# Kernel optimization log

Measured on AMD Instinct MI355X. Metric: run time of the kernel, lower is better.

The kernel has to match this reference:

```python
import jax, jax.numpy as jnp
import numpy as np

jax.config.update("jax_enable_x64", True)  # torch casts to double for matrix_exp

EPS_DIAG = 1e-6


def setup_inputs() -> dict:
    key = jax.random.key(0)
    B, D, NB, S = 32, 128, 8, 128
    ks = jax.random.split(key, 9)
    return {
        "z0r": jax.random.normal(ks[0], (B, D), jnp.float32),
        "z0i": jax.random.normal(ks[1], (B, D), jnp.float32),
        # uniform grid: dt = time_steps[0] = 0.01, diffs == dt (uniform branch)
        "time_steps": (jnp.arange(S, dtype=jnp.float32) + 1.0) * 0.01,
        "k_coeffs": jax.random.normal(ks[2], (B, NB), jnp.float32),
        "r_coeffs": jax.random.normal(ks[3], (B, NB), jnp.float32),
        "alpha": jax.random.normal(ks[4], (B, 1), jnp.float32),
        "beta": jax.random.normal(ks[5], (B, 1), jnp.float32),
        "K_bases": jax.random.normal(ks[6], (NB, D, D), jnp.float32) * 0.01,
        "R_bases": jax.random.normal(ks[7], (NB, D, D), jnp.float32) * 0.01,
    }


def _build_generator(k_coeffs, r_coeffs, alpha, beta, K_bases, R_bases):
    # A = alpha * skew(K_sum) + beta * -(R_sum^T @ R_sum), per batch element
    K_sum = jnp.einsum("bn,nij->bij", k_coeffs, K_bases)
    R_sum = jnp.einsum("bn,nij->bij", r_coeffs, R_bases)
    skew = K_sum - jnp.swapaxes(K_sum, -1, -2)
    neg_gram = -jnp.einsum("bji,bjk->bik", R_sum, R_sum)  # -(R^T @ R)
    return alpha[..., None] * skew + beta[..., None] * neg_gram  # (B, D, D)


def _propagators(A, time_steps, uniform):
    D = A.shape[-1]
    S = time_steps.shape[0]
    if uniform:
        dt = time_steps[0]
        A64 = A.astype(jnp.float64) * dt.astype(jnp.float64) + EPS_DIAG * jnp.eye(D, dtype=jnp.float64)
        M = jax.vmap(jax.scipy.linalg.expm)(A64).astype(jnp.complex64)  # (B, D, D)
        # cumulative matrix powers M, M^2, ..., M^S via O(log S) associative scan
        Ms = jnp.broadcast_to(M[:, None], (M.shape[0], S, D, D))
        props = jax.lax.associative_scan(jnp.matmul, Ms, axis=1)
    else:
        A_t = A[:, None].astype(jnp.float64) * time_steps.astype(jnp.float64)[None, :, None, None]
        props = jax.vmap(jax.vmap(jax.scipy.linalg.expm))(A_t).astype(jnp.complex64)
    return props  # (B, S, D, D)


def reference(z0r, z0i, time_steps, k_coeffs, r_coeffs, alpha, beta, K_bases, R_bases):
    ts = np.asarray(time_steps)
    uniform = ts.shape[0] <= 1 or np.allclose(ts[1:] - ts[:-1], ts[0], atol=1e-6)
    A = _build_generator(k_coeffs, r_coeffs, alpha, beta, K_bases, R_bases)
    props = _propagators(A, time_steps, uniform)
    z = (z0r + 1j * z0i).astype(jnp.complex64)  # (B, D)
    # z_evolved[b, s, o] = sum_i z[b, i] * props[b, s, o, i]
    return jnp.einsum("bi,bsoi->bso", z, props)
```

## Files before the change

### kernel.cpp

```cpp
#include <hip/hip_runtime.h>

#define BATCH   32
#define DIM     128
#define NBASES  8
#define SSTEPS  128
#define LDA     136

typedef __attribute__((ext_vector_type(8)))  short s8v;
typedef __attribute__((ext_vector_type(4)))  short s4v;
typedef __attribute__((ext_vector_type(4)))  float f4v;
typedef __attribute__((ext_vector_type(16))) float f16v;

__device__ __forceinline__ f4v mf(s8v a, s8v b, f4v c) {
    return __builtin_amdgcn_mfma_f32_16x16x32_bf16(a, b, c, 0, 0, 0);
}
__device__ __forceinline__ f16v mf32(s8v a, s8v b, f16v c) {
    return __builtin_amdgcn_mfma_f32_32x32x16_bf16(a, b, c, 0, 0, 0);
}
__device__ __forceinline__ s8v ld8(const short* p) {
    return *reinterpret_cast<const s8v*>(p);
}
__device__ __forceinline__ s4v ld4(const short* p) {
    return *reinterpret_cast<const s4v*>(p);
}
__device__ __forceinline__ void st4(short* p, s4v v) {
    *reinterpret_cast<s4v*>(p) = v;
}
__device__ __forceinline__ float upbf(short h) {
    return __uint_as_float(((unsigned)(unsigned short)h) << 16);
}
__device__ __forceinline__ void splitbf(float v, short& hi, short& lo) {
    const unsigned u = __float_as_uint(v);
    hi = (short)(u >> 16);
    const float fh = __uint_as_float(u & 0xffff0000u);
    lo = (short)(__float_as_uint(v - fh) >> 16);
}

__device__ __forceinline__ void write_out(float* __restrict__ outF, int b, int sidx,
                                          int o, int c, float val,
                                          int interleaved, int out_size)
{
    if (interleaved) {
        const int oi = ((b * SSTEPS + sidx) * DIM + o) * 2 + c;
        if (oi < out_size) outF[oi] = val;
    } else if (c == 0) {
        const int oi = (b * SSTEPS + sidx) * DIM + o;
        if (oi < out_size) outF[oi] = val;
    }
}

template<bool TRO, bool NMO>
__device__ __forceinline__ void mm32(const short* __restrict__ Ah,
                                     const short* __restrict__ Al,
                                     const short* __restrict__ Bh,
                                     const short* __restrict__ Bl,
                                     f16v& acc, f16v& acct,
                                     int mb, int nb, int lane)
{
    const int l31 = lane & 31, koc = (lane >> 5) * 8;
    #pragma unroll
    for (int ks = 0; ks < 8; ++ks) {
        const int ko = ks * 16 + koc;
        const s8v ah = ld8(Ah + (mb + l31) * LDA + ko);
        const s8v al = ld8(Al + (mb + l31) * LDA + ko);
        const s8v bh = ld8(Bh + (nb + l31) * LDA + ko);
        const s8v bl = ld8(Bl + (nb + l31) * LDA + ko);
        if (TRO) {
            acc = mf32(ah, bh, acc);
            acc = mf32(ah, bl, acc);
            acc = mf32(al, bh, acc);
        }
        if (NMO) {
            acct = mf32(bh, ah, acct);
            acct = mf32(bl, ah, acct);
            acct = mf32(bh, al, acct);
        }
    }
}

__global__ __launch_bounds__(256)
void sum_kr(const float* __restrict__ kco, const float* __restrict__ rco,
            const float* __restrict__ KB,  const float* __restrict__ RB,
            float* __restrict__ ws)
{
    const int b = blockIdx.x >> 3, s = blockIdx.x & 7, t = threadIdx.x;
    const int boff = s * 16 * DIM + t * 8;
    const int r = s * 16 + (t >> 4), c = (t & 15) * 8;
    float kc[NBASES], rc[NBASES];
    #pragma unroll
    for (int n = 0; n < NBASES; ++n) {
        kc[n] = kco[b * NBASES + n];
        rc[n] = rco[b * NBASES + n];
    }
    float4 ka = {0.f,0.f,0.f,0.f}, kb4 = {0.f,0.f,0.f,0.f};
    float4 ra = {0.f,0.f,0.f,0.f}, rb4 = {0.f,0.f,0.f,0.f};
    #pragma unroll
    for (int n = 0; n < NBASES; ++n) {
        const float4 k0 = *reinterpret_cast<const float4*>(KB + n * DIM * DIM + boff);
        const float4 k1 = *reinterpret_cast<const float4*>(KB + n * DIM * DIM + boff + 4);
        const float4 r0 = *reinterpret_cast<const float4*>(RB + n * DIM * DIM + boff);
        const float4 r1 = *reinterpret_cast<const float4*>(RB + n * DIM * DIM + boff + 4);
        ka.x += kc[n] * k0.x; ka.y += kc[n] * k0.y; ka.z += kc[n] * k0.z; ka.w += kc[n] * k0.w;
        kb4.x += kc[n] * k1.x; kb4.y += kc[n] * k1.y; kb4.z += kc[n] * k1.z; kb4.w += kc[n] * k1.w;
        ra.x += rc[n] * r0.x; ra.y += rc[n] * r0.y; ra.z += rc[n] * r0.z; ra.w += rc[n] * r0.w;
        rb4.x += rc[n] * r1.x; rb4.y += rc[n] * r1.y; rb4.z += rc[n] * r1.z; rb4.w += rc[n] * r1.w;
    }
    float* Ks  = ws + (size_t)b * DIM * DIM;
    float* KsT = ws + (size_t)BATCH * DIM * DIM + (size_t)b * DIM * DIM;
    float* RsT = ws + (size_t)2 * BATCH * DIM * DIM + (size_t)b * DIM * DIM;
    *reinterpret_cast<float4*>(Ks + boff)     = ka;
    *reinterpret_cast<float4*>(Ks + boff + 4) = kb4;
    const float kv[8] = {ka.x, ka.y, ka.z, ka.w, kb4.x, kb4.y, kb4.z, kb4.w};
    const float rv[8] = {ra.x, ra.y, ra.z, ra.w, rb4.x, rb4.y, rb4.z, rb4.w};
    #pragma unroll
    for (int j = 0; j < 8; ++j) {
        KsT[(c + j) * DIM + r] = kv[j];
        RsT[(c + j) * DIM + r] = rv[j];
    }
}

template<int PRE>
__global__ __launch_bounds__(1024) __attribute__((amdgpu_waves_per_eu(4, 4)))
void htg_mfma(const float* __restrict__ z0r, const float* __restrict__ z0i,
              const float* __restrict__ ts,  const float* __restrict__ kco,
              const float* __restrict__ rco, const float* __restrict__ alp,
              const float* __restrict__ bet, const float* __restrict__ KB,
              const float* __restrict__ RB,  const float* __restrict__ wsum,
              float* __restrict__ outF, int interleaved, int out_size)
{
    __shared__ short nm_hi[DIM * LDA], nm_lo[DIM * LDA];
    __shared__ short tr_hi[DIM * LDA], tr_lo[DIM * LDA];
    __shared__ short ht_hi[32 * LDA],  ht_lo[32 * LDA];

    const int b = blockIdx.x, t = threadIdx.x;
    const int w = t >> 6, lane = t & 63;
    const int l15 = lane & 15, quad = lane >> 4;
    const int l31 = lane & 31, kq = lane >> 5;
    const f4v z4 = {0.f, 0.f, 0.f, 0.f};
    const int mb = (w & 3) * 32, nb = (w >> 2) * 32;

    if (PRE) {
        const float* RsT = wsum + (size_t)2 * BATCH * DIM * DIM + (size_t)b * DIM * DIM;
        #pragma unroll
        for (int q = 0; q < 4; ++q) {
            const int e = q * 4096 + t * 4;
            const float4 rv = *reinterpret_cast<const float4*>(RsT + e);
            const int row = e >> 7, colr = e & 127;
            const float rr[4] = {rv.x, rv.y, rv.z, rv.w};
            s4v h4, l4;
            #pragma unroll
            for (int j = 0; j < 4; ++j) {
                short hi, lo; splitbf(rr[j], hi, lo);
                h4[j] = hi; l4[j] = lo;
            }
            st4(&tr_hi[row * LDA + colr], h4);
            st4(&tr_lo[row * LDA + colr], l4);
        }
        if (t < 2 * DIM) {
            const int c = t >> 7, o = t & 127;
            const float zv = (c == 0) ? z0r[b * DIM + o] : z0i[b * DIM + o];
            short hi, lo; splitbf(zv, hi, lo);
            ht_hi[c * LDA + o] = hi; ht_lo[c * LDA + o] = lo;
        }
    } else {
        float rc[NBASES], kc[NBASES];
        #pragma unroll
        for (int n = 0; n < NBASES; ++n) {
            rc[n] = rco[b * NBASES + n];
            kc[n] = kco[b * NBASES + n];
        }
        #pragma unroll
        for (int q = 0; q < 4; ++q) {
            const int e = q * 4096 + t * 4;
            float4 r4 = {0.f, 0.f, 0.f, 0.f}, k4 = {0.f, 0.f, 0.f, 0.f};
            #pragma unroll
            for (int n = 0; n < NBASES; ++n) {
                const float4 rvv = *reinterpret_cast<const float4*>(RB + n * DIM * DIM + e);
                const float4 kvv = *reinterpret_cast<const float4*>(KB + n * DIM * DIM + e);
                r4.x += rc[n] * rvv.x; r4.y += rc[n] * rvv.y;
                r4.z += rc[n] * rvv.z; r4.w += rc[n] * rvv.w;
                k4.x += kc[n] * kvv.x; k4.y += kc[n] * kvv.y;
                k4.z += kc[n] * kvv.z; k4.w += kc[n] * kvv.w;
            }
            const int r = e >> 7, c = e & 127;
            const float rr[4] = {r4.x, r4.y, r4.z, r4.w};
            const float kk[4] = {k4.x, k4.y, k4.z, k4.w};
            s4v kh, kl;
            #pragma unroll
            for (int j = 0; j < 4; ++j) {
                short hi, lo;
                splitbf(rr[j], hi, lo);
                tr_hi[(c + j) * LDA + r] = hi; tr_lo[(c + j) * LDA + r] = lo;
                splitbf(kk[j], hi, lo);
                kh[j] = hi; kl[j] = lo;
            }
            st4(&nm_hi[r * LDA + c], kh);
            st4(&nm_lo[r * LDA + c], kl);
        }
        if (t < 2 * DIM) {
            const int c = t >> 7, o = t & 127;
            const float zv = (c == 0) ? z0r[b * DIM + o] : z0i[b * DIM + o];
            short hi, lo; splitbf(zv, hi, lo);
            ht_hi[c * LDA + o] = hi; ht_lo[c * LDA + o] = lo;
        }
    }
    __syncthreads();

    f16v acc, acct;
    float xsave[16], xsaveT[16];

    float kd[4][4], kdT[4][4];
    if (PRE) {
        const float* Ks  = wsum + (size_t)b * DIM * DIM;
        const float* KsT = wsum + (size_t)BATCH * DIM * DIM + (size_t)b * DIM * DIM;
        #pragma unroll
        for (int r4 = 0; r4 < 4; ++r4) {
            const int row0 = mb + 8 * r4 + 4 * kq;
            const int col  = nb + l31;
            const int rt0  = nb + 8 * r4 + 4 * kq;
            const int ct   = mb + l31;
            #pragma unroll
            for (int j = 0; j < 4; ++j) {
                kd[r4][j]  = Ks[(row0 + j) * DIM + col] - KsT[(row0 + j) * DIM + col];
                kdT[r4][j] = KsT[(rt0 + j) * DIM + ct]  - Ks[(rt0 + j) * DIM + ct];
            }
        }
    } else {
        #pragma unroll
        for (int r4 = 0; r4 < 4; ++r4) {
            {
                const int row0 = mb + 8 * r4 + 4 * kq;
                const int col  = nb + l31;
                const s4v k2h = ld4(&nm_hi[col * LDA + row0]);
                const s4v k2l = ld4(&nm_lo[col * LDA + row0]);
                #pragma unroll
                for (int j = 0; j < 4; ++j)
                    kd[r4][j] = (upbf(nm_hi[(row0 + j) * LDA + col]) +
                                 upbf(nm_lo[(row0 + j) * LDA + col]))
                              - (upbf(k2h[j]) + upbf(k2l[j]));
            }
            {
                const int rt0 = nb + 8 * r4 + 4 * kq;
                const int ct  = mb + l31;
                const s4v k1h = ld4(&nm_hi[ct * LDA + rt0]);
                const s4v k1l = ld4(&nm_lo[ct * LDA + rt0]);
                #pragma unroll
                for (int j = 0; j < 4; ++j)
                    kdT[r4][j] = (upbf(k1h[j]) + upbf(k1l[j]))
                               - (upbf(nm_hi[(rt0 + j) * LDA + ct]) +
                                  upbf(nm_lo[(rt0 + j) * LDA + ct]));
            }
        }
    }
    #pragma unroll
    for (int i = 0; i < 16; ++i) { acc[i] = 0.f; acct[i] = 0.f; }
    mm32<true, true>(tr_hi, tr_lo, tr_hi, tr_lo, acc, acct, mb, nb, lane);
    __syncthreads();
    {
        const float alpha = alp[b], beta = bet[b], dtf = ts[0];
        #pragma unroll
        for (int r4 = 0; r4 < 4; ++r4) {
            {
                const int row0 = mb + 8 * r4 + 4 * kq;
                const int col  = nb + l31;
                s4v h4, l4;
                #pragma unroll
                for (int j = 0; j < 4; ++j) {
                    float x = (alpha * kd[r4][j] - beta * acc[4 * r4 + j]) * dtf;
                    if (row0 + j == col) x += 1e-6f;
                    xsave[4 * r4 + j] = x;
                    short hi, lo; splitbf(x, hi, lo);
                    h4[j] = hi; l4[j] = lo;
                }
                st4(&tr_hi[col * LDA + row0], h4);
                st4(&tr_lo[col * LDA + row0], l4);
            }
            {
                const int rt0 = nb + 8 * r4 + 4 * kq;
                const int ct  = mb + l31;
                s4v h4, l4;
                #pragma unroll
                for (int j = 0; j < 4; ++j) {
                    float x = (alpha * kdT[r4][j] - beta * acct[4 * r4 + j]) * dtf;
                    if (ct == rt0 + j) x += 1e-6f;
                    xsaveT[4 * r4 + j] = x;
                    short hi, lo; splitbf(x, hi, lo);
                    h4[j] = hi; l4[j] = lo;
                }
                st4(&nm_hi[ct * LDA + rt0], h4);
                st4(&nm_lo[ct * LDA + rt0], l4);
            }
        }
    }
    __syncthreads();

    #pragma unroll
    for (int i = 0; i < 16; ++i) { acc[i] = 0.f; acct[i] = 0.f; }
    mm32<true, true>(nm_hi, nm_lo, tr_hi, tr_lo, acc, acct, mb, nb, lane);
    __syncthreads();
    #pragma unroll
    for (int r4 = 0; r4 < 4; ++r4) {
        {
            const int row0 = mb + 8 * r4 + 4 * kq;
            const int col  = nb + l31;
            s4v h4, l4;
            #pragma unroll
            for (int j = 0; j < 4; ++j) {
                const float m = ((row0 + j == col) ? 1.f : 0.f)
                              + xsave[4 * r4 + j] + 0.5f * acc[4 * r4 + j];
                short hi, lo; splitbf(m, hi, lo);
                h4[j] = hi; l4[j] = lo;
            }
            st4(&tr_hi[col * LDA + row0], h4);
            st4(&tr_lo[col * LDA + row0], l4);
        }
        {
            const int rt0 = nb + 8 * r4 + 4 * kq;
            const int ct  = mb + l31;
            s4v h4, l4;
            #pragma unroll
            for (int j = 0; j < 4; ++j) {
                const float m = ((ct == rt0 + j) ? 1.f : 0.f)
                              + xsaveT[4 * r4 + j] + 0.5f * acct[4 * r4 + j];
                short hi, lo; splitbf(m, hi, lo);
                h4[j] = hi; l4[j] = lo;
            }
            st4(&nm_hi[ct * LDA + rt0], h4);
            st4(&nm_lo[ct * LDA + rt0], l4);
        }
    }
    __syncthreads();

    float arp[4];

    #pragma unroll
    for (int stage = 0; stage < 3; ++stage) {
        const int J = 1 << stage;
        if (stage > 0) {
            const int Jp = J >> 1;
            if (w < 8 && l15 < 2 * Jp) {
                const int o0 = w * 16 + quad * 4;
                const int sidx = (l15 >> 1) + Jp - 1;
                #pragma unroll
                for (int r = 0; r < 4; ++r)
                    write_out(outF, b, sidx, o0 + r, l15 & 1, arp[r],
                              interleaved, out_size);
            }
        }
        f4v ar = z4;
        #pragma unroll
        for (int i = 0; i < 16; ++i) { acc[i] = 0.f; acct[i] = 0.f; }
        if (w < 8) {
            #pragma unroll
            for (int kk = 0; kk < DIM; kk += 32) {
                const int ko = kk + quad * 8;
                const s8v rah = ld8(nm_hi + (w * 16 + l15) * LDA + ko);
                const s8v ral = ld8(nm_lo + (w * 16 + l15) * LDA + ko);
                const s8v rbh = ld8(ht_hi + l15 * LDA + ko);
                const s8v rbl = ld8(ht_lo + l15 * LDA + ko);
                ar = mf(rah, rbh, ar);
                ar = mf(rah, rbl, ar);
                ar = mf(ral, rbh, ar);
            }
        }
        mm32<true, true>(nm_hi, nm_lo, tr_hi, tr_lo, acc, acct, mb, nb, lane);
        __syncthreads();
        if (w < 8 && l15 < 2 * J) {
            const int o0 = w * 16 + quad * 4;
            s4v h4, l4;
            #pragma unroll
            for (int r = 0; r < 4; ++r) {
                short hi, lo; splitbf(ar[r], hi, lo);
                h4[r] = hi; l4[r] = lo;
            }
            st4(&ht_hi[(l15 + 2 * J) * LDA + o0], h4);
            st4(&ht_lo[(l15 + 2 * J) * LDA + o0], l4);
        }
        #pragma unroll
        for (int r = 0; r < 4; ++r) arp[r] = ar[r];
        #pragma unroll
        for (int r4 = 0; r4 < 4; ++r4) {
            {
                const int row0 = mb + 8 * r4 + 4 * kq;
                const int col  = nb + l31;
                s4v h4, l4;
                #pragma unroll
                for (int j = 0; j < 4; ++j) {
                    short hi, lo; splitbf(acc[4 * r4 + j], hi, lo);
                    h4[j] = hi; l4[j] = lo;
                }
                st4(&tr_hi[col * LDA + row0], h4);
                st4(&tr_lo[col * LDA + row0], l4);
            }
            {
                const int rt0 = nb + 8 * r4 + 4 * kq;
                const int ct  = mb + l31;
                s4v h4, l4;
                #pragma unroll
                for (int j = 0; j < 4; ++j) {
                    short hi, lo; splitbf(acct[4 * r4 + j], hi, lo);
                    h4[j] = hi; l4[j] = lo;
                }
                st4(&nm_hi[ct * LDA + rt0], h4);
                st4(&nm_lo[ct * LDA + rt0], l4);
            }
        }
        __syncthreads();
    }

    {
        const int J = 8;
        {
            const int Jp = 4;
            if (w < 8 && l15 < 2 * Jp) {
                const int o0 = w * 16 + quad * 4;
                const int sidx = (l15 >> 1) + Jp - 1;
                #pragma unroll
                for (int r = 0; r < 4; ++r)
                    write_out(outF, b, sidx, o0 + r, l15 & 1, arp[r],
                              interleaved, out_size);
            }
        }
        f4v ar = z4;
        #pragma unroll
        for (int i = 0; i < 16; ++i) acct[i] = 0.f;
        if (w < 8) {
            #pragma unroll
            for (int kk = 0; kk < DIM; kk += 32) {
                const int ko = kk + quad * 8;
                const s8v rah = ld8(nm_hi + (w * 16 + l15) * LDA + ko);
                const s8v ral = ld8(nm_lo + (w * 16 + l15) * LDA + ko);
                const s8v rbh = ld8(ht_hi + l15 * LDA + ko);
                const s8v rbl = ld8(ht_lo + l15 * LDA + ko);
                ar = mf(rah, rbh, ar);
                ar = mf(rah, rbl, ar);
                ar = mf(ral, rbh, ar);
            }
        }
        mm32<false, true>(nm_hi, nm_lo, tr_hi, tr_lo, acc, acct, mb, nb, lane);
        __syncthreads();
        if (w < 8 && l15 < 2 * J) {
            const int o0 = w * 16 + quad * 4;
            s4v h4, l4;
            #pragma unroll
            for (int r = 0; r < 4; ++r) {
                short hi, lo; splitbf(ar[r], hi, lo);
                h4[r] = hi; l4[r] = lo;
            }
            st4(&ht_hi[(l15 + 2 * J) * LDA + o0], h4);
            st4(&ht_lo[(l15 + 2 * J) * LDA + o0], l4);
        }
        #pragma unroll
        for (int r = 0; r < 4; ++r) arp[r] = ar[r];
        #pragma unroll
        for (int r4 = 0; r4 < 4; ++r4) {
            const int rt0 = nb + 8 * r4 + 4 * kq;
            const int ct  = mb + l31;
            s4v h4, l4;
            #pragma unroll
            for (int j = 0; j < 4; ++j) {
                short hi, lo; splitbf(acct[4 * r4 + j], hi, lo);
                h4[j] = hi; l4[j] = lo;
            }
            st4(&nm_hi[ct * LDA + rt0], h4);
            st4(&nm_lo[ct * LDA + rt0], l4);
        }
        __syncthreads();
    }

    {
        const int Jp = 8;
        if (w < 8 && l15 < 2 * Jp) {
            const int o0 = w * 16 + quad * 4;
            const int sidx = (l15 >> 1) + Jp - 1;
            #pragma unroll
            for (int r = 0; r < 4; ++r)
                write_out(outF, b, sidx, o0 + r, l15 & 1, arp[r],
                          interleaved, out_size);
        }
    }

    const int sw = w >> 1, ct = w & 1;
    s8v vah[4], val[4];
    #pragma unroll
    for (int k4 = 0; k4 < 4; ++k4) {
        const int ko = k4 * 32 + quad * 8;
        vah[k4] = ld8(nm_hi + (sw * 16 + l15) * LDA + ko);
        val[k4] = ld8(nm_lo + (sw * 16 + l15) * LDA + ko);
    }
    float wprev[4];
    short *rh_hi = ht_hi, *rh_lo = ht_lo;
    short *wh_hi = tr_hi, *wh_lo = tr_lo;
    #pragma unroll
    for (int q = 1; q <= 8; ++q) {
        if (q > 1) {
            const int o0 = sw * 16 + quad * 4;
            const int n = ct * 16 + l15;
            const int sidx = 16 * (q - 1) + (n >> 1) - 1;
            if (sidx < SSTEPS) {
                #pragma unroll
                for (int r = 0; r < 4; ++r)
                    write_out(outF, b, sidx, o0 + r, n & 1, wprev[r],
                              interleaved, out_size);
            }
        }
        f4v a2 = z4;
        #pragma unroll
        for (int k4 = 0; k4 < 4; ++k4) {
            const int ko = k4 * 32 + quad * 8;
            const s8v bh = ld8(rh_hi + (ct * 16 + l15) * LDA + ko);
            const s8v bl = ld8(rh_lo + (ct * 16 + l15) * LDA + ko);
            a2 = mf(vah[k4], bh, a2);
            a2 = mf(vah[k4], bl, a2);
            a2 = mf(val[k4], bh, a2);
        }
        #pragma unroll
        for (int r = 0; r < 4; ++r) wprev[r] = a2[r];
        if (q < 8) {
            const int o0 = sw * 16 + quad * 4;
            const int n = ct * 16 + l15;
            s4v h4, l4;
            #pragma unroll
            for (int r = 0; r < 4; ++r) {
                short hi, lo; splitbf(a2[r], hi, lo);
                h4[r] = hi; l4[r] = lo;
            }
            st4(&wh_hi[n * LDA + o0], h4);
            st4(&wh_lo[n * LDA + o0], l4);
            __syncthreads();
        }
        short* tp;
        tp = rh_hi; rh_hi = wh_hi; wh_hi = tp;
        tp = rh_lo; rh_lo = wh_lo; wh_lo = tp;
    }
    {
        const int o0 = sw * 16 + quad * 4;
        const int n = ct * 16 + l15;
        const int sidx = 128 + (n >> 1) - 1;
        if (sidx < SSTEPS) {
            #pragma unroll
            for (int r = 0; r < 4; ++r)
                write_out(outF, b, sidx, o0 + r, n & 1, wprev[r],
                          interleaved, out_size);
        }
    }
}

extern "C" void kernel_launch(void* const* d_in, const int* in_sizes, int n_in,
                              void* d_out, int out_size, void* d_ws, size_t ws_size,
                              hipStream_t stream)
{
    (void)in_sizes; (void)n_in;
    const float* z0r = (const float*)d_in[0];
    const float* z0i = (const float*)d_in[1];
    const float* ts  = (const float*)d_in[2];
    const float* kco = (const float*)d_in[3];
    const float* rco = (const float*)d_in[4];
    const float* alp = (const float*)d_in[5];
    const float* bet = (const float*)d_in[6];
    const float* KB  = (const float*)d_in[7];
    const float* RB  = (const float*)d_in[8];
    float* outF = (float*)d_out;

    const int interleaved = (out_size >= 2 * BATCH * SSTEPS * DIM) ? 1 : 0;
    const size_t ws_needed = (size_t)3 * BATCH * DIM * DIM * sizeof(float);

    if (d_ws != nullptr && ws_size >= ws_needed) {
        float* ws = (float*)d_ws;
        sum_kr<<<dim3(BATCH * 8), dim3(256), 0, stream>>>(kco, rco, KB, RB, ws);
        htg_mfma<1><<<dim3(BATCH), dim3(1024), 0, stream>>>(
            z0r, z0i, ts, kco, rco, alp, bet, KB, RB, ws, outF, interleaved, out_size);
    } else {
        htg_mfma<0><<<dim3(BATCH), dim3(1024), 0, stream>>>(
            z0r, z0i, ts, kco, rco, alp, bet, KB, RB, nullptr, outF, interleaved, out_size);
    }
}
```

Baseline: 112.7 us.

## Coalesce transposed writes via LDS and presplit R^T to bf16 hi/lo

The sum kernel now stages the K and R partial sums in shared memory so the transposed stores to global memory are coalesced vector writes instead of strided scalar writes. It also writes R^T already split into bf16 hi/lo halves, so the main kernel can copy them straight into LDS with 16-byte loads instead of converting in place. The main kernel moves the K-difference global loads earlier and writes the transposed-generator tile to LDS before the barrier, which removes one barrier-separated phase. The cost is an extra LDS round trip and barrier in the sum kernel, and the workspace layout changes (12 bytes per element).

```diff
diff --git a/kernel.cpp b/kernel.cpp
--- a/kernel.cpp
+++ b/kernel.cpp
@@ -25,6 +25,9 @@
 }
 __device__ __forceinline__ void st4(short* p, s4v v) {
     *reinterpret_cast<s4v*>(p) = v;
+}
+__device__ __forceinline__ void st8(short* p, s8v v) {
+    *reinterpret_cast<s8v*>(p) = v;
 }
 __device__ __forceinline__ float upbf(short h) {
     return __uint_as_float(((unsigned)(unsigned short)h) << 16);
@@ -83,9 +86,10 @@
             const float* __restrict__ KB,  const float* __restrict__ RB,
             float* __restrict__ ws)
 {
+    __shared__ float sk[16][129], sr[16][129];
     const int b = blockIdx.x >> 3, s = blockIdx.x & 7, t = threadIdx.x;
-    const int boff = s * 16 * DIM + t * 8;
-    const int r = s * 16 + (t >> 4), c = (t & 15) * 8;
+    const int rl = t >> 4, c0 = (t & 15) * 8;
+    const int boff = (s * 16 + rl) * DIM + c0;
     float kc[NBASES], rc[NBASES];
     #pragma unroll
     for (int n = 0; n < NBASES; ++n) {
@@ -107,15 +111,48 @@
     }
     float* Ks  = ws + (size_t)b * DIM * DIM;
     float* KsT = ws + (size_t)BATCH * DIM * DIM + (size_t)b * DIM * DIM;
-    float* RsT = ws + (size_t)2 * BATCH * DIM * DIM + (size_t)b * DIM * DIM;
+    unsigned short* RTh = reinterpret_cast<unsigned short*>(ws + (size_t)2 * BATCH * DIM * DIM)
+                        + (size_t)b * DIM * DIM;
+    unsigned short* RTl = RTh + (size_t)BATCH * DIM * DIM;
+
     *reinterpret_cast<float4*>(Ks + boff)     = ka;
     *reinterpret_cast<float4*>(Ks + boff + 4) = kb4;
+
     const float kv[8] = {ka.x, ka.y, ka.z, ka.w, kb4.x, kb4.y, kb4.z, kb4.w};
     const float rv[8] = {ra.x, ra.y, ra.z, ra.w, rb4.x, rb4.y, rb4.z, rb4.w};
     #pragma unroll
     for (int j = 0; j < 8; ++j) {
-        KsT[(c + j) * DIM + r] = kv[j];
-        RsT[(c + j) * DIM + r] = rv[j];
+        sk[rl][c0 + j] = kv[j];
+        sr[rl][c0 + j] = rv[j];
+    }
+    __syncthreads();
+    if (t < 128) {
+        const int c = t;
+        float tmp[16];
+        #pragma unroll
+        for (int i = 0; i < 16; ++i) tmp[i] = sk[i][c];
+        float* dst = KsT + (size_t)c * DIM + 16 * s;
+        #pragma unroll
+        for (int j = 0; j < 4; ++j)
+            *reinterpret_cast<float4*>(dst + 4 * j) =
+                make_float4(tmp[4*j], tmp[4*j+1], tmp[4*j+2], tmp[4*j+3]);
+    } else {
+        const int c = t - 128;
+        s8v h0, h1, l0, l1;
+        #pragma unroll
+        for (int i = 0; i < 8; ++i) {
+            short hi, lo;
+            splitbf(sr[i][c], hi, lo);
+            h0[i] = hi; l0[i] = lo;
+            splitbf(sr[i + 8][c], hi, lo);
+            h1[i] = hi; l1[i] = lo;
+        }
+        short* dh = reinterpret_cast<short*>(RTh) + (size_t)c * DIM + 16 * s;
+        short* dl = reinterpret_cast<short*>(RTl) + (size_t)c * DIM + 16 * s;
+        *reinterpret_cast<s8v*>(dh)     = h0;
+        *reinterpret_cast<s8v*>(dh + 8) = h1;
+        *reinterpret_cast<s8v*>(dl)     = l0;
+        *reinterpret_cast<s8v*>(dl + 8) = l1;
     }
 }
 
@@ -139,23 +176,35 @@
     const f4v z4 = {0.f, 0.f, 0.f, 0.f};
     const int mb = (w & 3) * 32, nb = (w >> 2) * 32;
 
+    const float alpha = alp[b], beta = bet[b], dtf = ts[0];
+
+    float kd[4][4], kdT[4][4];
     if (PRE) {
-        const float* RsT = wsum + (size_t)2 * BATCH * DIM * DIM + (size_t)b * DIM * DIM;
-        #pragma unroll
-        for (int q = 0; q < 4; ++q) {
-            const int e = q * 4096 + t * 4;
-            const float4 rv = *reinterpret_cast<const float4*>(RsT + e);
-            const int row = e >> 7, colr = e & 127;
-            const float rr[4] = {rv.x, rv.y, rv.z, rv.w};
-            s4v h4, l4;
-            #pragma unroll
-            for (int j = 0; j < 4; ++j) {
-                short hi, lo; splitbf(rr[j], hi, lo);
-                h4[j] = hi; l4[j] = lo;
-            }
-            st4(&tr_hi[row * LDA + colr], h4);
-            st4(&tr_lo[row * LDA + colr], l4);
-        }
+        const float* Ks  = wsum + (size_t)b * DIM * DIM;
+        const float* KsT = wsum + (size_t)BATCH * DIM * DIM + (size_t)b * DIM * DIM;
+        #pragma unroll
+        for (int r4 = 0; r4 < 4; ++r4) {
+            const int row0 = mb + 8 * r4 + 4 * kq;
+            const int col  = nb + l31;
+            const int rt0  = nb + 8 * r4 + 4 * kq;
+            const int ct   = mb + l31;
+            #pragma unroll
+            for (int j = 0; j < 4; ++j) {
+                kd[r4][j]  = Ks[(row0 + j) * DIM + col] - KsT[(row0 + j) * DIM + col];
+                kdT[r4][j] = KsT[(rt0 + j) * DIM + ct]  - Ks[(rt0 + j) * DIM + ct];
+            }
+        }
+    }
+
+    if (PRE) {
+        const short* RTh = reinterpret_cast<const short*>(wsum + (size_t)2 * BATCH * DIM * DIM)
+                         + (size_t)b * DIM * DIM;
+        const short* RTl = RTh + (size_t)BATCH * DIM * DIM;
+        const int row = t >> 3, cs = (t & 7) * 16;
+        st8(&tr_hi[row * LDA + cs],     ld8(RTh + row * DIM + cs));
+        st8(&tr_hi[row * LDA + cs + 8], ld8(RTh + row * DIM + cs + 8));
+        st8(&tr_lo[row * LDA + cs],     ld8(RTl + row * DIM + cs));
+        st8(&tr_lo[row * LDA + cs + 8], ld8(RTl + row * DIM + cs + 8));
         if (t < 2 * DIM) {
             const int c = t >> 7, o = t & 127;
             const float zv = (c == 0) ? z0r[b * DIM + o] : z0i[b * DIM + o];
@@ -209,23 +258,7 @@
     f16v acc, acct;
     float xsave[16], xsaveT[16];
 
-    float kd[4][4], kdT[4][4];
-    if (PRE) {
-        const float* Ks  = wsum + (size_t)b * DIM * DIM;
-        const float* KsT = wsum + (size_t)BATCH * DIM * DIM + (size_t)b * DIM * DIM;
-        #pragma unroll
-        for (int r4 = 0; r4 < 4; ++r4) {
-            const int row0 = mb + 8 * r4 + 4 * kq;
-            const int col  = nb + l31;
-            const int rt0  = nb + 8 * r4 + 4 * kq;
-            const int ct   = mb + l31;
-            #pragma unroll
-            for (int j = 0; j < 4; ++j) {
-                kd[r4][j]  = Ks[(row0 + j) * DIM + col] - KsT[(row0 + j) * DIM + col];
-                kdT[r4][j] = KsT[(rt0 + j) * DIM + ct]  - Ks[(rt0 + j) * DIM + ct];
-            }
-        }
-    } else {
+    if (!PRE) {
         #pragma unroll
         for (int r4 = 0; r4 < 4; ++r4) {
             {
@@ -252,44 +285,64 @@
             }
         }
     }
+
     #pragma unroll
     for (int i = 0; i < 16; ++i) { acc[i] = 0.f; acct[i] = 0.f; }
     mm32<true, true>(tr_hi, tr_lo, tr_hi, tr_lo, acc, acct, mb, nb, lane);
+
+    if (PRE) {
+        #pragma unroll
+        for (int r4 = 0; r4 < 4; ++r4) {
+            const int rt0 = nb + 8 * r4 + 4 * kq;
+            const int ct  = mb + l31;
+            s4v h4, l4;
+            #pragma unroll
+            for (int j = 0; j < 4; ++j) {
+                float x = (alpha * kdT[r4][j] - beta * acct[4 * r4 + j]) * dtf;
+                if (ct == rt0 + j) x += 1e-6f;
+                xsaveT[4 * r4 + j] = x;
+                short hi, lo; splitbf(x, hi, lo);
+                h4[j] = hi; l4[j] = lo;
+            }
+            st4(&nm_hi[ct * LDA + rt0], h4);
+            st4(&nm_lo[ct * LDA + rt0], l4);
+        }
+    }
     __syncthreads();
+    if (!PRE) {
+        #pragma unroll
+        for (int r4 = 0; r4 < 4; ++r4) {
+            const int rt0 = nb + 8 * r4 + 4 * kq;
+            const int ct  = mb + l31;
+            s4v h4, l4;
+            #pragma unroll
+            for (int j = 0; j < 4; ++j) {
+                float x = (alpha * kdT[r4][j] - beta * acct[4 * r4 + j]) * dtf;
+                if (ct == rt0 + j) x += 1e-6f;
+                xsaveT[4 * r4 + j] = x;
+                short hi, lo; splitbf(x, hi, lo);
+                h4[j] = hi; l4[j] = lo;
+            }
+            st4(&nm_hi[ct * LDA + rt0], h4);
+            st4(&nm_lo[ct * LDA + rt0], l4);
+        }
+    }
     {
-        const float alpha = alp[b], beta = bet[b], dtf = ts[0];
         #pragma unroll
         for (int r4 = 0; r4 < 4; ++r4) {
-            {
-                const int row0 = mb + 8 * r4 + 4 * kq;
-                const int col  = nb + l31;
-                s4v h4, l4;
-                #pragma unroll
-                for (int j = 0; j < 4; ++j) {
-                    float x = (alpha * kd[r4][j] - beta * acc[4 * r4 + j]) * dtf;
-                    if (row0 + j == col) x += 1e-6f;
-                    xsave[4 * r4 + j] = x;
-                    short hi, lo; splitbf(x, hi, lo);
-                    h4[j] = hi; l4[j] = lo;
-                }
-                st4(&tr_hi[col * LDA + row0], h4);
-                st4(&tr_lo[col * LDA + row0], l4);
-            }
-            {
-                const int rt0 = nb + 8 * r4 + 4 * kq;
-                const int ct  = mb + l31;
-                s4v h4, l4;
-                #pragma unroll
-                for (int j = 0; j < 4; ++j) {
-                    float x = (alpha * kdT[r4][j] - beta * acct[4 * r4 + j]) * dtf;
-                    if (ct == rt0 + j) x += 1e-6f;
-                    xsaveT[4 * r4 + j] = x;
-                    short hi, lo; splitbf(x, hi, lo);
-                    h4[j] = hi; l4[j] = lo;
-                }
-                st4(&nm_hi[ct * LDA + rt0], h4);
-                st4(&nm_lo[ct * LDA + rt0], l4);
-            }
+            const int row0 = mb + 8 * r4 + 4 * kq;
+            const int col  = nb + l31;
+            s4v h4, l4;
+            #pragma unroll
+            for (int j = 0; j < 4; ++j) {
+                float x = (alpha * kd[r4][j] - beta * acc[4 * r4 + j]) * dtf;
+                if (row0 + j == col) x += 1e-6f;
+                xsave[4 * r4 + j] = x;
+                short hi, lo; splitbf(x, hi, lo);
+                h4[j] = hi; l4[j] = lo;
+            }
+            st4(&tr_hi[col * LDA + row0], h4);
+            st4(&tr_lo[col * LDA + row0], l4);
         }
     }
     __syncthreads();
@@ -563,7 +616,7 @@
     float* outF = (float*)d_out;
 
     const int interleaved = (out_size >= 2 * BATCH * SSTEPS * DIM) ? 1 : 0;
-    const size_t ws_needed = (size_t)3 * BATCH * DIM * DIM * sizeof(float);
+    const size_t ws_needed = (size_t)BATCH * DIM * DIM * 12;
 
     if (d_ws != nullptr && ws_size >= ws_needed) {
         float* ws = (float*)d_ws;
```

After: 112.9 us. No clear change (+0.2%).
